# Performance work log

Hardware: AMD Instinct MI355X
Metric: run time of the kernel (lower is better)

The kernel has to match this reference:

```python
import jax, jax.numpy as jnp
import numpy as np

NUM_HEADS = 16


def spike(x):
    # forward of SpikeFunction: Heaviside step
    return (x > 0).astype(x.dtype)


def setup_inputs() -> dict:
    key = jax.random.key(0)
    ks = jax.random.split(key, 11)
    B, S, D = 2, 2048, 1024
    s = 1.0 / np.sqrt(D)
    return {
        "query": jax.random.normal(ks[0], (B, S, D), jnp.float32),
        "key": jax.random.normal(ks[1], (B, S, D), jnp.float32),
        "value": jax.random.normal(ks[2], (B, S, D), jnp.float32),
        "Wq": jax.random.normal(ks[3], (D, D), jnp.float32) * s,
        "bq": jnp.zeros((D,), jnp.float32),
        "Wk": jax.random.normal(ks[4], (D, D), jnp.float32) * s,
        "bk": jnp.zeros((D,), jnp.float32),
        "Wv": jax.random.normal(ks[5], (D, D), jnp.float32) * s,
        "bv": jnp.zeros((D,), jnp.float32),
        "Wo": jax.random.normal(ks[6], (D, D), jnp.float32) * s,
        "bo": jnp.zeros((D,), jnp.float32),
    }


def reference(query, key, value, Wq, bq, Wk, bk, Wv, bv, Wo, bo):
    B, S, D = query.shape
    H = NUM_HEADS
    hd = D // H
    # torch Linear: x @ W.T + b
    q = (query @ Wq.T + bq).reshape(B, S, H, hd).transpose(0, 2, 1, 3)
    k = (key @ Wk.T + bk).reshape(B, S, H, hd).transpose(0, 2, 1, 3)
    v = (value @ Wv.T + bv).reshape(B, S, H, hd).transpose(0, 2, 1, 3)
    scale = 1.0 / np.sqrt(hd).astype(np.float32)
    scores = jnp.einsum('bhqd,bhkd->bhqk', q, k) * scale  # [B,H,S,S]
    attn = spike(scores)  # elementwise threshold instead of softmax
    ctx = jnp.einsum('bhqk,bhkd->bhqd', attn, v)
    ctx = ctx.transpose(0, 2, 1, 3).reshape(B, S, D)
    out = ctx @ Wo.T + bo
    return out, attn
```

## Files before the change

kernel.cpp:

```cpp
#include <hip/hip_runtime.h>


#define SEQ 2048
#define DIM 1024
#define NH 16
#define HD 64
#define BATCH 2
#define MROWS (BATCH * SEQ)
#define BHT (BATCH * NH)

typedef __attribute__((ext_vector_type(8))) short short8;
typedef __attribute__((ext_vector_type(4))) float f4;
typedef unsigned short ushort;

__device__ __forceinline__ f4 mfma16(short8 a, short8 b, f4 c) {
    return __builtin_amdgcn_mfma_f32_16x16x32_bf16(a, b, c, 0, 0, 0);
}
__device__ __forceinline__ ushort rne16(float x) {
    union { float f; unsigned u; } a; a.f = x;
    return (ushort)((a.u + 0x7fffu + ((a.u >> 16) & 1u)) >> 16);
}
__device__ __forceinline__ void split2(float x, ushort& h, ushort& l) {
    union { float f; unsigned u; } a; a.f = x;
    unsigned hu = a.u & 0xffff0000u;
    h = (ushort)(hu >> 16);
    union { unsigned u; float f; } hb; hb.u = hu;
    l = rne16(x - hb.f);
}
__device__ __forceinline__ short8 ld8(const ushort* p) { return *(const short8*)p; }

__global__ __launch_bounds__(256) void wconv(const float* __restrict__ Wq,
                                             const float* __restrict__ Wk,
                                             const float* __restrict__ Wv,
                                             const float* __restrict__ Wo,
                                             ushort* __restrict__ Wqh, ushort* __restrict__ Wql,
                                             ushort* __restrict__ Wkh, ushort* __restrict__ Wkl,
                                             ushort* __restrict__ Wvb, ushort* __restrict__ Wob) {
    int i = (blockIdx.x * 256 + threadIdx.x) * 4;
    int job = blockIdx.y;
    const float* src = job == 0 ? Wq : job == 1 ? Wk : job == 2 ? Wv : Wo;
    float4 w = *(const float4*)&src[i];
    float xs[4] = {w.x, w.y, w.z, w.w};
    if (job < 2) {
        ushort h[4], l[4];
#pragma unroll
        for (int j = 0; j < 4; ++j) split2(xs[j], h[j], l[j]);
        ushort* ph = job ? Wkh : Wqh;
        ushort* pl = job ? Wkl : Wql;
        *(short4*)&ph[i] = make_short4(h[0], h[1], h[2], h[3]);
        *(short4*)&pl[i] = make_short4(l[0], l[1], l[2], l[3]);
    } else {
        ushort* po = job == 2 ? Wvb : Wob;
        *(short4*)&po[i] = make_short4(rne16(xs[0]), rne16(xs[1]), rne16(xs[2]), rne16(xs[3]));
    }
}

template <int B>
__device__ __forceinline__ void ld_qk(const float* __restrict__ X, const ushort* __restrict__ Wh,
                                      const ushort* __restrict__ Wl, int m0, int n0, int la, int qd,
                                      int k0, float4 (&xA)[2][2][2], short8 (&wH)[2][4],
                                      short8 (&wL)[2][4]) {
#pragma unroll
    for (int ms = 0; ms < 2; ++ms) {
        const float* ap = &X[(size_t)(m0 + ms * 16 + la) * DIM + k0 + qd * 8];
        xA[B][ms][0] = *(const float4*)ap;
        xA[B][ms][1] = *(const float4*)(ap + 4);
    }
#pragma unroll
    for (int ns = 0; ns < 4; ++ns) {
        size_t wi = (size_t)(n0 + ns * 16 + la) * DIM + k0 + qd * 8;
        wH[B][ns] = ld8(&Wh[wi]);
        wL[B][ns] = ld8(&Wl[wi]);
    }
}

template <int B>
__device__ __forceinline__ void fma_qk(float4 (&xA)[2][2][2], short8 (&wH)[2][4],
                                       short8 (&wL)[2][4], f4 (&acc)[2][4]) {
    short8 ahi[2], alo[2];
#pragma unroll
    for (int ms = 0; ms < 2; ++ms) {
        float xs[8] = {xA[B][ms][0].x, xA[B][ms][0].y, xA[B][ms][0].z, xA[B][ms][0].w,
                       xA[B][ms][1].x, xA[B][ms][1].y, xA[B][ms][1].z, xA[B][ms][1].w};
#pragma unroll
        for (int j = 0; j < 8; ++j) {
            ushort h, l;
            split2(xs[j], h, l);
            ahi[ms][j] = (short)h;
            alo[ms][j] = (short)l;
        }
    }
#pragma unroll
    for (int ns = 0; ns < 4; ++ns)
#pragma unroll
        for (int ms = 0; ms < 2; ++ms) {
            acc[ms][ns] = mfma16(alo[ms], wH[B][ns], acc[ms][ns]);
            acc[ms][ns] = mfma16(ahi[ms], wL[B][ns], acc[ms][ns]);
            acc[ms][ns] = mfma16(ahi[ms], wH[B][ns], acc[ms][ns]);
        }
}

template <int B>
__device__ __forceinline__ void ld_v(const float* __restrict__ X, const ushort* __restrict__ Wb,
                                     int m0, int n0, int la, int qd, int k0,
                                     float4 (&xA)[2][2][2], short8 (&wH)[2][4]) {
#pragma unroll
    for (int ms = 0; ms < 2; ++ms) {
        const float* ap = &X[(size_t)(m0 + ms * 16 + la) * DIM + k0 + qd * 8];
        xA[B][ms][0] = *(const float4*)ap;
        xA[B][ms][1] = *(const float4*)(ap + 4);
    }
#pragma unroll
    for (int ns = 0; ns < 4; ++ns)
        wH[B][ns] = ld8(&Wb[(size_t)(n0 + ns * 16 + la) * DIM + k0 + qd * 8]);
}

template <int B>
__device__ __forceinline__ void fma_v(float4 (&xA)[2][2][2], short8 (&wH)[2][4], f4 (&acc)[2][4]) {
    short8 a[2];
#pragma unroll
    for (int ms = 0; ms < 2; ++ms) {
        float xs[8] = {xA[B][ms][0].x, xA[B][ms][0].y, xA[B][ms][0].z, xA[B][ms][0].w,
                       xA[B][ms][1].x, xA[B][ms][1].y, xA[B][ms][1].z, xA[B][ms][1].w};
#pragma unroll
        for (int j = 0; j < 8; ++j) a[ms][j] = (short)rne16(xs[j]);
    }
#pragma unroll
    for (int ns = 0; ns < 4; ++ns)
#pragma unroll
        for (int ms = 0; ms < 2; ++ms) acc[ms][ns] = mfma16(a[ms], wH[B][ns], acc[ms][ns]);
}

__global__ __launch_bounds__(256, 2) void proj_qkv(
    const float* __restrict__ query, const float* __restrict__ key, const float* __restrict__ value,
    const ushort* __restrict__ Wqh, const ushort* __restrict__ Wql,
    const ushort* __restrict__ Wkh, const ushort* __restrict__ Wkl,
    const ushort* __restrict__ Wvb,
    const float* __restrict__ bq, const float* __restrict__ bk, const float* __restrict__ bv,
    ushort* __restrict__ Qhi, ushort* __restrict__ Qlo,
    ushort* __restrict__ Khi, ushort* __restrict__ Klo, ushort* __restrict__ Vt) {
    const int z = blockIdx.z;
    const int t = threadIdx.x, wave = t >> 6, lane = t & 63;
    const int la = lane & 15, qd = lane >> 4;
    const int m0 = blockIdx.x * 128 + wave * 32;
    const int n0 = blockIdx.y * 64;

    float4 xA[2][2][2];
    short8 wH[2][4], wL[2][4];
    f4 acc[2][4] = {};

    if (z < 2) {
        const float* X = z ? key : query;
        const ushort* Wh = z ? Wkh : Wqh;
        const ushort* Wl = z ? Wkl : Wql;
        ld_qk<0>(X, Wh, Wl, m0, n0, la, qd, 0, xA, wH, wL);
        for (int k0 = 0; k0 < DIM; k0 += 64) {
            ld_qk<1>(X, Wh, Wl, m0, n0, la, qd, k0 + 32, xA, wH, wL);
            fma_qk<0>(xA, wH, wL, acc);
            ld_qk<0>(X, Wh, Wl, m0, n0, la, qd, (k0 + 64) & (DIM - 1), xA, wH, wL);
            fma_qk<1>(xA, wH, wL, acc);
        }
        const float* bias = z ? bk : bq;
        ushort* Oh = z ? Khi : Qhi;
        ushort* Ol = z ? Klo : Qlo;
#pragma unroll
        for (int ns = 0; ns < 4; ++ns) {
            int n = n0 + ns * 16 + la;
            float bvv = bias[n];
            int h = n >> 6, d = n & 63;
#pragma unroll
            for (int ms = 0; ms < 2; ++ms)
#pragma unroll
                for (int r = 0; r < 4; ++r) {
                    int m = m0 + ms * 16 + qd * 4 + r;
                    int b = m >> 11, s = m & 2047;
                    ushort hh, ll;
                    split2(acc[ms][ns][r] + bvv, hh, ll);
                    size_t o = ((size_t)(b * NH + h) * SEQ + s) * HD + d;
                    Oh[o] = hh;
                    Ol[o] = ll;
                }
        }
    } else {
        __shared__ ushort Ts[4][64][40];
        ld_v<0>(value, Wvb, m0, n0, la, qd, 0, xA, wH);
        for (int k0 = 0; k0 < DIM; k0 += 64) {
            ld_v<1>(value, Wvb, m0, n0, la, qd, k0 + 32, xA, wH);
            fma_v<0>(xA, wH, acc);
            ld_v<0>(value, Wvb, m0, n0, la, qd, (k0 + 64) & (DIM - 1), xA, wH);
            fma_v<1>(xA, wH, acc);
        }
#pragma unroll
        for (int ns = 0; ns < 4; ++ns) {
            float bvv = bv[n0 + ns * 16 + la];
#pragma unroll
            for (int ms = 0; ms < 2; ++ms)
#pragma unroll
                for (int r = 0; r < 4; ++r)
                    Ts[wave][ns * 16 + la][ms * 16 + qd * 4 + r] = rne16(acc[ms][ns][r] + bvv);
        }
        int b = m0 >> 11, s0 = m0 & 2047, h = n0 >> 6;
        size_t vbase = (size_t)(b * NH + h) * HD * SEQ;
#pragma unroll
        for (int it = 0; it < 4; ++it) {
            int d = it * 16 + (lane >> 2), sc = (lane & 3) * 8;
            short8 v0 = *(const short8*)&Ts[wave][d][sc];
            *(short8*)&Vt[vbase + (size_t)d * SEQ + s0 + sc] = v0;
        }
    }
}

template <int B>
__device__ __forceinline__ void ld_at(const ushort* __restrict__ Khi, const ushort* __restrict__ Klo,
                                      const ushort* __restrict__ Vt, int bh, int c0, int la, int qd,
                                      short8 (&kH)[2][2][2], short8 (&kL)[2][2][2],
                                      short8 (&vB)[2][4]) {
#pragma unroll
    for (int n2 = 0; n2 < 2; ++n2)
#pragma unroll
        for (int ks = 0; ks < 2; ++ks) {
            size_t ki = ((size_t)bh * SEQ + c0 + n2 * 16 + la) * HD + ks * 32 + qd * 8;
            kH[B][n2][ks] = ld8(&Khi[ki]);
            kL[B][n2][ks] = ld8(&Klo[ki]);
        }
#pragma unroll
    for (int ns = 0; ns < 4; ++ns)
        vB[B][ns] = ld8(&Vt[((size_t)bh * HD + ns * 16 + la) * SEQ + c0 + qd * 8]);
}

template <int B>
__device__ __forceinline__ void half_at(ushort (*Ps)[40], float* __restrict__ attn,
                                        int bh, int q0, int c0, int wave, int lane, int la, int qd,
                                        short8 (&qhi)[2][2], short8 (&qlo)[2][2],
                                        short8 (&kH)[2][2][2], short8 (&kL)[2][2][2],
                                        short8 (&vB)[2][4], f4 (&cacc)[2][4]) {
    f4 s[2][2] = {};
#pragma unroll
    for (int n2 = 0; n2 < 2; ++n2)
#pragma unroll
        for (int ks = 0; ks < 2; ++ks)
#pragma unroll
            for (int ms = 0; ms < 2; ++ms) {
                s[ms][n2] = mfma16(qlo[ms][ks], kH[B][n2][ks], s[ms][n2]);
                s[ms][n2] = mfma16(qhi[ms][ks], kL[B][n2][ks], s[ms][n2]);
                s[ms][n2] = mfma16(qhi[ms][ks], kH[B][n2][ks], s[ms][n2]);
            }
#pragma unroll
    for (int ms = 0; ms < 2; ++ms)
#pragma unroll
        for (int n2 = 0; n2 < 2; ++n2)
#pragma unroll
            for (int r = 0; r < 4; ++r)
                Ps[wave * 32 + ms * 16 + qd * 4 + r][n2 * 16 + la] =
                    s[ms][n2][r] > 0.f ? (ushort)0x3f80 : (ushort)0;
#pragma unroll
    for (int it = 0; it < 4; ++it) {
        int row = it * 8 + (lane >> 3);
        short4 p = *(const short4*)&Ps[wave * 32 + row][(lane & 7) * 4];
        float4 o;
        o.x = __uint_as_float(((unsigned)(ushort)p.x) << 16);
        o.y = __uint_as_float(((unsigned)(ushort)p.y) << 16);
        o.z = __uint_as_float(((unsigned)(ushort)p.z) << 16);
        o.w = __uint_as_float(((unsigned)(ushort)p.w) << 16);
        *(float4*)&attn[((size_t)bh * SEQ + q0 + row) * SEQ + c0 + (lane & 7) * 4] = o;
    }
    short8 pa[2];
#pragma unroll
    for (int ms = 0; ms < 2; ++ms)
        pa[ms] = *(const short8*)&Ps[wave * 32 + ms * 16 + la][qd * 8];
#pragma unroll
    for (int ns = 0; ns < 4; ++ns)
#pragma unroll
        for (int ms = 0; ms < 2; ++ms) cacc[ms][ns] = mfma16(pa[ms], vB[B][ns], cacc[ms][ns]);
}

__global__ __launch_bounds__(256, 2) void attn_mfma(
    const ushort* __restrict__ Qhi, const ushort* __restrict__ Qlo,
    const ushort* __restrict__ Khi, const ushort* __restrict__ Klo,
    const ushort* __restrict__ Vt, float* __restrict__ attn, ushort* __restrict__ ctxb) {
    __shared__ ushort Ps[128][40];
    const int t = threadIdx.x, wave = t >> 6, lane = t & 63;
    const int la = lane & 15, qd = lane >> 4;
    const int bh = blockIdx.x;
    const int q0 = blockIdx.y * 128 + wave * 32;

    short8 qhi[2][2], qlo[2][2];
#pragma unroll
    for (int ms = 0; ms < 2; ++ms)
#pragma unroll
        for (int ks = 0; ks < 2; ++ks) {
            size_t qi = ((size_t)bh * SEQ + q0 + ms * 16 + la) * HD + ks * 32 + qd * 8;
            qhi[ms][ks] = ld8(&Qhi[qi]);
            qlo[ms][ks] = ld8(&Qlo[qi]);
        }

    short8 kH[2][2][2], kL[2][2][2], vB[2][4];
    f4 cacc[2][4] = {};
    ld_at<0>(Khi, Klo, Vt, bh, 0, la, qd, kH, kL, vB);
    for (int h = 0; h < 64; h += 2) {
        ld_at<1>(Khi, Klo, Vt, bh, (h + 1) * 32, la, qd, kH, kL, vB);
        half_at<0>(Ps, attn, bh, q0, h * 32, wave, lane, la, qd, qhi, qlo, kH, kL, vB, cacc);
        ld_at<0>(Khi, Klo, Vt, bh, ((h + 2) & 63) * 32, la, qd, kH, kL, vB);
        half_at<1>(Ps, attn, bh, q0, (h + 1) * 32, wave, lane, la, qd, qhi, qlo, kH, kL, vB, cacc);
    }
#pragma unroll
    for (int ns = 0; ns < 4; ++ns)
#pragma unroll
        for (int ms = 0; ms < 2; ++ms)
#pragma unroll
            for (int r = 0; r < 4; ++r) {
                int qrow = q0 + ms * 16 + qd * 4 + r;
                ctxb[((size_t)bh * SEQ + qrow) * HD + ns * 16 + la] = rne16(cacc[ms][ns][r]);
            }
}

template <int B>
__device__ __forceinline__ void ld_o(const ushort* __restrict__ Ctx, const ushort* __restrict__ Wb,
                                     int m0, int n0, int la, int qd, int k0,
                                     short8 (&aO)[2][2], short8 (&wO)[2][4]) {
#pragma unroll
    for (int ms = 0; ms < 2; ++ms) {
        int m = m0 + ms * 16 + la;
        int b = m >> 11, s = m & 2047;
        int k = k0 + qd * 8;
        int h = k >> 6, d = k & 63;
        aO[B][ms] = ld8(&Ctx[((size_t)(b * NH + h) * SEQ + s) * HD + d]);
    }
#pragma unroll
    for (int ns = 0; ns < 4; ++ns)
        wO[B][ns] = ld8(&Wb[(size_t)(n0 + ns * 16 + la) * DIM + k0 + qd * 8]);
}

__global__ __launch_bounds__(256, 2) void proj_out(const ushort* __restrict__ Ctx,
                                                   const ushort* __restrict__ Wb,
                                                   const float* __restrict__ bias,
                                                   float* __restrict__ out) {
    const int t = threadIdx.x, wave = t >> 6, lane = t & 63;
    const int la = lane & 15, qd = lane >> 4;
    const int m0 = blockIdx.x * 128 + wave * 32;
    const int n0 = blockIdx.y * 64;

    short8 aO[2][2], wO[2][4];
    f4 acc[2][4] = {};
    ld_o<0>(Ctx, Wb, m0, n0, la, qd, 0, aO, wO);
    for (int k0 = 0; k0 < DIM; k0 += 64) {
        ld_o<1>(Ctx, Wb, m0, n0, la, qd, k0 + 32, aO, wO);
#pragma unroll
        for (int ns = 0; ns < 4; ++ns)
#pragma unroll
            for (int ms = 0; ms < 2; ++ms) acc[ms][ns] = mfma16(aO[0][ms], wO[0][ns], acc[ms][ns]);
        ld_o<0>(Ctx, Wb, m0, n0, la, qd, (k0 + 64) & (DIM - 1), aO, wO);
#pragma unroll
        for (int ns = 0; ns < 4; ++ns)
#pragma unroll
            for (int ms = 0; ms < 2; ++ms) acc[ms][ns] = mfma16(aO[1][ms], wO[1][ns], acc[ms][ns]);
    }
#pragma unroll
    for (int ns = 0; ns < 4; ++ns) {
        int n = n0 + ns * 16 + la;
        float bvv = bias[n];
#pragma unroll
        for (int ms = 0; ms < 2; ++ms)
#pragma unroll
            for (int r = 0; r < 4; ++r) {
                int m = m0 + ms * 16 + qd * 4 + r;
                out[(size_t)m * DIM + n] = acc[ms][ns][r] + bvv;
            }
    }
}

extern "C" void kernel_launch(void* const* d_in, const int* in_sizes, int n_in,
                              void* d_out, int out_size, void* d_ws, size_t ws_size,
                              hipStream_t stream) {
    const float* query = (const float*)d_in[0];
    const float* key   = (const float*)d_in[1];
    const float* value = (const float*)d_in[2];
    const float* Wq = (const float*)d_in[3];
    const float* bq = (const float*)d_in[4];
    const float* Wk = (const float*)d_in[5];
    const float* bk = (const float*)d_in[6];
    const float* Wv = (const float*)d_in[7];
    const float* bv = (const float*)d_in[8];
    const float* Wo = (const float*)d_in[9];
    const float* bo = (const float*)d_in[10];

    float* out  = (float*)d_out;
    float* attn = out + (size_t)MROWS * DIM;

    const size_t NE = (size_t)MROWS * DIM;
    const size_t WE = (size_t)DIM * DIM;
    ushort* Qhi = (ushort*)d_ws;
    ushort* Qlo = Qhi + NE;
    ushort* Khi = Qlo + NE;
    ushort* Klo = Khi + NE;
    ushort* Vt  = Klo + NE;
    ushort* Wqh = Vt + NE;
    ushort* Wql = Wqh + WE;
    ushort* Wkh = Wql + WE;
    ushort* Wkl = Wkh + WE;
    ushort* Wvb = Wkl + WE;
    ushort* Wob = Wvb + WE;
    ushort* Ctx = Wqh;

    dim3 blk(256);
    hipLaunchKernelGGL(wconv, dim3(WE / 1024, 4), blk, 0, stream,
                       Wq, Wk, Wv, Wo, Wqh, Wql, Wkh, Wkl, Wvb, Wob);
    hipLaunchKernelGGL(proj_qkv, dim3(32, 16, 3), blk, 0, stream,
                       query, key, value, Wqh, Wql, Wkh, Wkl, Wvb, bq, bk, bv,
                       Qhi, Qlo, Khi, Klo, Vt);
    hipLaunchKernelGGL(attn_mfma, dim3(32, 16), blk, 0, stream,
                       Qhi, Qlo, Khi, Klo, Vt, attn, Ctx);
    hipLaunchKernelGGL(proj_out, dim3(32, 16), blk, 0, stream, Ctx, Wob, bo, out);
}
```

Measured before the change: 1.042 ms.

## Fuse all four stages into one persistent kernel with grid-wide barriers

Replaces the four kernels (weight conversion, QKV projection, attention, output projection) with one persistent 512-block kernel. The stages are separated by atomic-counter grid barriers that a small init kernel resets. The aim is to remove launch gaps and kernel-boundary drains. The QKV stage now runs Q, K and V sequentially in each block instead of spreading them over 1536 blocks, which lowers parallelism in that stage. The design also depends on all 512 blocks being co-resident, or the barriers deadlock.

```diff
diff --git a/kernel.cpp b/kernel.cpp
--- a/kernel.cpp
+++ b/kernel.cpp
@@ -7,7 +7,7 @@
 #define HD 64
 #define BATCH 2
 #define MROWS (BATCH * SEQ)
-#define BHT (BATCH * NH)
+#define NBLK 512
 
 typedef __attribute__((ext_vector_type(8))) short short8;
 typedef __attribute__((ext_vector_type(4))) float f4;
@@ -29,30 +29,21 @@
 }
 __device__ __forceinline__ short8 ld8(const ushort* p) { return *(const short8*)p; }
 
-__global__ __launch_bounds__(256) void wconv(const float* __restrict__ Wq,
-                                             const float* __restrict__ Wk,
-                                             const float* __restrict__ Wv,
-                                             const float* __restrict__ Wo,
-                                             ushort* __restrict__ Wqh, ushort* __restrict__ Wql,
-                                             ushort* __restrict__ Wkh, ushort* __restrict__ Wkl,
-                                             ushort* __restrict__ Wvb, ushort* __restrict__ Wob) {
-    int i = (blockIdx.x * 256 + threadIdx.x) * 4;
-    int job = blockIdx.y;
-    const float* src = job == 0 ? Wq : job == 1 ? Wk : job == 2 ? Wv : Wo;
-    float4 w = *(const float4*)&src[i];
-    float xs[4] = {w.x, w.y, w.z, w.w};
-    if (job < 2) {
-        ushort h[4], l[4];
-#pragma unroll
-        for (int j = 0; j < 4; ++j) split2(xs[j], h[j], l[j]);
-        ushort* ph = job ? Wkh : Wqh;
-        ushort* pl = job ? Wkl : Wql;
-        *(short4*)&ph[i] = make_short4(h[0], h[1], h[2], h[3]);
-        *(short4*)&pl[i] = make_short4(l[0], l[1], l[2], l[3]);
-    } else {
-        ushort* po = job == 2 ? Wvb : Wob;
-        *(short4*)&po[i] = make_short4(rne16(xs[0]), rne16(xs[1]), rne16(xs[2]), rne16(xs[3]));
-    }
+__device__ __forceinline__ void gbar(unsigned* c) {
+    __builtin_amdgcn_fence(__ATOMIC_RELEASE, "agent");
+    __syncthreads();
+    if (threadIdx.x == 0) {
+        __hip_atomic_fetch_add(c, 1u, __ATOMIC_ACQ_REL, __HIP_MEMORY_SCOPE_AGENT);
+        while (__hip_atomic_load(c, __ATOMIC_ACQUIRE, __HIP_MEMORY_SCOPE_AGENT) < NBLK) {
+            __builtin_amdgcn_s_sleep(2);
+        }
+    }
+    __syncthreads();
+    __builtin_amdgcn_fence(__ATOMIC_ACQUIRE, "agent");
+}
+
+__global__ void init_barriers(unsigned* bar) {
+    if (threadIdx.x < 8) bar[threadIdx.x] = 0;
 }
 
 template <int B>
@@ -129,85 +120,6 @@
     for (int ns = 0; ns < 4; ++ns)
 #pragma unroll
         for (int ms = 0; ms < 2; ++ms) acc[ms][ns] = mfma16(a[ms], wH[B][ns], acc[ms][ns]);
-}
-
-__global__ __launch_bounds__(256, 2) void proj_qkv(
-    const float* __restrict__ query, const float* __restrict__ key, const float* __restrict__ value,
-    const ushort* __restrict__ Wqh, const ushort* __restrict__ Wql,
-    const ushort* __restrict__ Wkh, const ushort* __restrict__ Wkl,
-    const ushort* __restrict__ Wvb,
-    const float* __restrict__ bq, const float* __restrict__ bk, const float* __restrict__ bv,
-    ushort* __restrict__ Qhi, ushort* __restrict__ Qlo,
-    ushort* __restrict__ Khi, ushort* __restrict__ Klo, ushort* __restrict__ Vt) {
-    const int z = blockIdx.z;
-    const int t = threadIdx.x, wave = t >> 6, lane = t & 63;
-    const int la = lane & 15, qd = lane >> 4;
-    const int m0 = blockIdx.x * 128 + wave * 32;
-    const int n0 = blockIdx.y * 64;
-
-    float4 xA[2][2][2];
-    short8 wH[2][4], wL[2][4];
-    f4 acc[2][4] = {};
-
-    if (z < 2) {
-        const float* X = z ? key : query;
-        const ushort* Wh = z ? Wkh : Wqh;
-        const ushort* Wl = z ? Wkl : Wql;
-        ld_qk<0>(X, Wh, Wl, m0, n0, la, qd, 0, xA, wH, wL);
-        for (int k0 = 0; k0 < DIM; k0 += 64) {
-            ld_qk<1>(X, Wh, Wl, m0, n0, la, qd, k0 + 32, xA, wH, wL);
-            fma_qk<0>(xA, wH, wL, acc);
-            ld_qk<0>(X, Wh, Wl, m0, n0, la, qd, (k0 + 64) & (DIM - 1), xA, wH, wL);
-            fma_qk<1>(xA, wH, wL, acc);
-        }
-        const float* bias = z ? bk : bq;
-        ushort* Oh = z ? Khi : Qhi;
-        ushort* Ol = z ? Klo : Qlo;
-#pragma unroll
-        for (int ns = 0; ns < 4; ++ns) {
-            int n = n0 + ns * 16 + la;
-            float bvv = bias[n];
-            int h = n >> 6, d = n & 63;
-#pragma unroll
-            for (int ms = 0; ms < 2; ++ms)
-#pragma unroll
-                for (int r = 0; r < 4; ++r) {
-                    int m = m0 + ms * 16 + qd * 4 + r;
-                    int b = m >> 11, s = m & 2047;
-                    ushort hh, ll;
-                    split2(acc[ms][ns][r] + bvv, hh, ll);
-                    size_t o = ((size_t)(b * NH + h) * SEQ + s) * HD + d;
-                    Oh[o] = hh;
-                    Ol[o] = ll;
-                }
-        }
-    } else {
-        __shared__ ushort Ts[4][64][40];
-        ld_v<0>(value, Wvb, m0, n0, la, qd, 0, xA, wH);
-        for (int k0 = 0; k0 < DIM; k0 += 64) {
-            ld_v<1>(value, Wvb, m0, n0, la, qd, k0 + 32, xA, wH);
-            fma_v<0>(xA, wH, acc);
-            ld_v<0>(value, Wvb, m0, n0, la, qd, (k0 + 64) & (DIM - 1), xA, wH);
-            fma_v<1>(xA, wH, acc);
-        }
-#pragma unroll
-        for (int ns = 0; ns < 4; ++ns) {
-            float bvv = bv[n0 + ns * 16 + la];
-#pragma unroll
-            for (int ms = 0; ms < 2; ++ms)
-#pragma unroll
-                for (int r = 0; r < 4; ++r)
-                    Ts[wave][ns * 16 + la][ms * 16 + qd * 4 + r] = rne16(acc[ms][ns][r] + bvv);
-        }
-        int b = m0 >> 11, s0 = m0 & 2047, h = n0 >> 6;
-        size_t vbase = (size_t)(b * NH + h) * HD * SEQ;
-#pragma unroll
-        for (int it = 0; it < 4; ++it) {
-            int d = it * 16 + (lane >> 2), sc = (lane & 3) * 8;
-            short8 v0 = *(const short8*)&Ts[wave][d][sc];
-            *(short8*)&Vt[vbase + (size_t)d * SEQ + s0 + sc] = v0;
-        }
-    }
 }
 
 template <int B>
@@ -274,46 +186,6 @@
         for (int ms = 0; ms < 2; ++ms) cacc[ms][ns] = mfma16(pa[ms], vB[B][ns], cacc[ms][ns]);
 }
 
-__global__ __launch_bounds__(256, 2) void attn_mfma(
-    const ushort* __restrict__ Qhi, const ushort* __restrict__ Qlo,
-    const ushort* __restrict__ Khi, const ushort* __restrict__ Klo,
-    const ushort* __restrict__ Vt, float* __restrict__ attn, ushort* __restrict__ ctxb) {
-    __shared__ ushort Ps[128][40];
-    const int t = threadIdx.x, wave = t >> 6, lane = t & 63;
-    const int la = lane & 15, qd = lane >> 4;
-    const int bh = blockIdx.x;
-    const int q0 = blockIdx.y * 128 + wave * 32;
-
-    short8 qhi[2][2], qlo[2][2];
-#pragma unroll
-    for (int ms = 0; ms < 2; ++ms)
-#pragma unroll
-        for (int ks = 0; ks < 2; ++ks) {
-            size_t qi = ((size_t)bh * SEQ + q0 + ms * 16 + la) * HD + ks * 32 + qd * 8;
-            qhi[ms][ks] = ld8(&Qhi[qi]);
-            qlo[ms][ks] = ld8(&Qlo[qi]);
-        }
-
-    short8 kH[2][2][2], kL[2][2][2], vB[2][4];
-    f4 cacc[2][4] = {};
-    ld_at<0>(Khi, Klo, Vt, bh, 0, la, qd, kH, kL, vB);
-    for (int h = 0; h < 64; h += 2) {
-        ld_at<1>(Khi, Klo, Vt, bh, (h + 1) * 32, la, qd, kH, kL, vB);
-        half_at<0>(Ps, attn, bh, q0, h * 32, wave, lane, la, qd, qhi, qlo, kH, kL, vB, cacc);
-        ld_at<0>(Khi, Klo, Vt, bh, ((h + 2) & 63) * 32, la, qd, kH, kL, vB);
-        half_at<1>(Ps, attn, bh, q0, (h + 1) * 32, wave, lane, la, qd, qhi, qlo, kH, kL, vB, cacc);
-    }
-#pragma unroll
-    for (int ns = 0; ns < 4; ++ns)
-#pragma unroll
-        for (int ms = 0; ms < 2; ++ms)
-#pragma unroll
-            for (int r = 0; r < 4; ++r) {
-                int qrow = q0 + ms * 16 + qd * 4 + r;
-                ctxb[((size_t)bh * SEQ + qrow) * HD + ns * 16 + la] = rne16(cacc[ms][ns][r]);
-            }
-}
-
 template <int B>
 __device__ __forceinline__ void ld_o(const ushort* __restrict__ Ctx, const ushort* __restrict__ Wb,
                                      int m0, int n0, int la, int qd, int k0,
@@ -331,41 +203,186 @@
         wO[B][ns] = ld8(&Wb[(size_t)(n0 + ns * 16 + la) * DIM + k0 + qd * 8]);
 }
 
-__global__ __launch_bounds__(256, 2) void proj_out(const ushort* __restrict__ Ctx,
-                                                   const ushort* __restrict__ Wb,
-                                                   const float* __restrict__ bias,
-                                                   float* __restrict__ out) {
+__global__ __launch_bounds__(256, 2) void mega(
+    const float* __restrict__ query, const float* __restrict__ key, const float* __restrict__ value,
+    const float* __restrict__ Wq, const float* __restrict__ bq,
+    const float* __restrict__ Wk, const float* __restrict__ bk,
+    const float* __restrict__ Wv, const float* __restrict__ bv,
+    const float* __restrict__ Wo, const float* __restrict__ bo,
+    float* __restrict__ out, float* __restrict__ attn,
+    ushort* __restrict__ Qhi, ushort* __restrict__ Qlo,
+    ushort* __restrict__ Khi, ushort* __restrict__ Klo,
+    ushort* __restrict__ Vt, ushort* __restrict__ Ctx,
+    ushort* __restrict__ Wqh, ushort* __restrict__ Wql,
+    ushort* __restrict__ Wkh, ushort* __restrict__ Wkl,
+    ushort* __restrict__ Wvb, ushort* __restrict__ Wob,
+    unsigned* __restrict__ bar) {
+    __shared__ ushort smem[10240];
     const int t = threadIdx.x, wave = t >> 6, lane = t & 63;
     const int la = lane & 15, qd = lane >> 4;
-    const int m0 = blockIdx.x * 128 + wave * 32;
-    const int n0 = blockIdx.y * 64;
-
-    short8 aO[2][2], wO[2][4];
-    f4 acc[2][4] = {};
-    ld_o<0>(Ctx, Wb, m0, n0, la, qd, 0, aO, wO);
-    for (int k0 = 0; k0 < DIM; k0 += 64) {
-        ld_o<1>(Ctx, Wb, m0, n0, la, qd, k0 + 32, aO, wO);
+    const int bid = blockIdx.x;
+
+    {
+#pragma unroll
+        for (int u = 0; u < 8; ++u) {
+            int unit = bid * 8 + u;
+            int mat = unit >> 10;
+            int i = (unit & 1023) * 1024 + t * 4;
+            const float* src = mat == 0 ? Wq : mat == 1 ? Wk : mat == 2 ? Wv : Wo;
+            float4 w = *(const float4*)&src[i];
+            float xs[4] = {w.x, w.y, w.z, w.w};
+            if (mat < 2) {
+                ushort h[4], l[4];
+#pragma unroll
+                for (int j = 0; j < 4; ++j) split2(xs[j], h[j], l[j]);
+                ushort* ph = mat ? Wkh : Wqh;
+                ushort* pl = mat ? Wkl : Wql;
+                *(short4*)&ph[i] = make_short4(h[0], h[1], h[2], h[3]);
+                *(short4*)&pl[i] = make_short4(l[0], l[1], l[2], l[3]);
+            } else {
+                ushort* po = mat == 2 ? Wvb : Wob;
+                *(short4*)&po[i] = make_short4(rne16(xs[0]), rne16(xs[1]), rne16(xs[2]), rne16(xs[3]));
+            }
+        }
+    }
+    gbar(bar + 0);
+
+    {
+        const int xb = bid & 31, yb = bid >> 5;
+        const int m0 = xb * 128 + wave * 32;
+        const int n0 = yb * 64;
+        float4 xA[2][2][2];
+        short8 wH[2][4], wL[2][4];
+#pragma unroll
+        for (int z = 0; z < 2; ++z) {
+            const float* X = z ? key : query;
+            const ushort* Wh = z ? Wkh : Wqh;
+            const ushort* Wl = z ? Wkl : Wql;
+            f4 acc[2][4] = {};
+            ld_qk<0>(X, Wh, Wl, m0, n0, la, qd, 0, xA, wH, wL);
+            for (int k0 = 0; k0 < DIM; k0 += 64) {
+                ld_qk<1>(X, Wh, Wl, m0, n0, la, qd, k0 + 32, xA, wH, wL);
+                fma_qk<0>(xA, wH, wL, acc);
+                ld_qk<0>(X, Wh, Wl, m0, n0, la, qd, (k0 + 64) & (DIM - 1), xA, wH, wL);
+                fma_qk<1>(xA, wH, wL, acc);
+            }
+            const float* bias = z ? bk : bq;
+            ushort* Oh = z ? Khi : Qhi;
+            ushort* Ol = z ? Klo : Qlo;
+#pragma unroll
+            for (int ns = 0; ns < 4; ++ns) {
+                int n = n0 + ns * 16 + la;
+                float bvv = bias[n];
+                int h = n >> 6, d = n & 63;
+#pragma unroll
+                for (int ms = 0; ms < 2; ++ms)
+#pragma unroll
+                    for (int r = 0; r < 4; ++r) {
+                        int m = m0 + ms * 16 + qd * 4 + r;
+                        int b = m >> 11, s = m & 2047;
+                        ushort hh, ll;
+                        split2(acc[ms][ns][r] + bvv, hh, ll);
+                        size_t o = ((size_t)(b * NH + h) * SEQ + s) * HD + d;
+                        Oh[o] = hh;
+                        Ol[o] = ll;
+                    }
+            }
+        }
+        {
+            ushort(*Ts)[64][40] = (ushort(*)[64][40])smem;
+            f4 acc[2][4] = {};
+            ld_v<0>(value, Wvb, m0, n0, la, qd, 0, xA, wH);
+            for (int k0 = 0; k0 < DIM; k0 += 64) {
+                ld_v<1>(value, Wvb, m0, n0, la, qd, k0 + 32, xA, wH);
+                fma_v<0>(xA, wH, acc);
+                ld_v<0>(value, Wvb, m0, n0, la, qd, (k0 + 64) & (DIM - 1), xA, wH);
+                fma_v<1>(xA, wH, acc);
+            }
+#pragma unroll
+            for (int ns = 0; ns < 4; ++ns) {
+                float bvv = bv[n0 + ns * 16 + la];
+#pragma unroll
+                for (int ms = 0; ms < 2; ++ms)
+#pragma unroll
+                    for (int r = 0; r < 4; ++r)
+                        Ts[wave][ns * 16 + la][ms * 16 + qd * 4 + r] = rne16(acc[ms][ns][r] + bvv);
+            }
+            int b = m0 >> 11, s0 = m0 & 2047, h = n0 >> 6;
+            size_t vbase = (size_t)(b * NH + h) * HD * SEQ;
+#pragma unroll
+            for (int it = 0; it < 4; ++it) {
+                int d = it * 16 + (lane >> 2), sc = (lane & 3) * 8;
+                short8 v0 = *(const short8*)&Ts[wave][d][sc];
+                *(short8*)&Vt[vbase + (size_t)d * SEQ + s0 + sc] = v0;
+            }
+        }
+    }
+    gbar(bar + 1);
+
+    {
+        ushort(*Ps)[40] = (ushort(*)[40])smem;
+        const int bh = bid & 31;
+        const int q0 = (bid >> 5) * 128 + wave * 32;
+        short8 qhi[2][2], qlo[2][2];
+#pragma unroll
+        for (int ms = 0; ms < 2; ++ms)
+#pragma unroll
+            for (int ks = 0; ks < 2; ++ks) {
+                size_t qi = ((size_t)bh * SEQ + q0 + ms * 16 + la) * HD + ks * 32 + qd * 8;
+                qhi[ms][ks] = ld8(&Qhi[qi]);
+                qlo[ms][ks] = ld8(&Qlo[qi]);
+            }
+        short8 kH[2][2][2], kL[2][2][2], vB[2][4];
+        f4 cacc[2][4] = {};
+        ld_at<0>(Khi, Klo, Vt, bh, 0, la, qd, kH, kL, vB);
+        for (int h = 0; h < 64; h += 2) {
+            ld_at<1>(Khi, Klo, Vt, bh, (h + 1) * 32, la, qd, kH, kL, vB);
+            half_at<0>(Ps, attn, bh, q0, h * 32, wave, lane, la, qd, qhi, qlo, kH, kL, vB, cacc);
+            ld_at<0>(Khi, Klo, Vt, bh, ((h + 2) & 63) * 32, la, qd, kH, kL, vB);
+            half_at<1>(Ps, attn, bh, q0, (h + 1) * 32, wave, lane, la, qd, qhi, qlo, kH, kL, vB, cacc);
+        }
 #pragma unroll
         for (int ns = 0; ns < 4; ++ns)
 #pragma unroll
-            for (int ms = 0; ms < 2; ++ms) acc[ms][ns] = mfma16(aO[0][ms], wO[0][ns], acc[ms][ns]);
-        ld_o<0>(Ctx, Wb, m0, n0, la, qd, (k0 + 64) & (DIM - 1), aO, wO);
-#pragma unroll
-        for (int ns = 0; ns < 4; ++ns)
-#pragma unroll
-            for (int ms = 0; ms < 2; ++ms) acc[ms][ns] = mfma16(aO[1][ms], wO[1][ns], acc[ms][ns]);
-    }
-#pragma unroll
-    for (int ns = 0; ns < 4; ++ns) {
-        int n = n0 + ns * 16 + la;
-        float bvv = bias[n];
-#pragma unroll
-        for (int ms = 0; ms < 2; ++ms)
-#pragma unroll
-            for (int r = 0; r < 4; ++r) {
-                int m = m0 + ms * 16 + qd * 4 + r;
-                out[(size_t)m * DIM + n] = acc[ms][ns][r] + bvv;
-            }
+            for (int ms = 0; ms < 2; ++ms)
+#pragma unroll
+                for (int r = 0; r < 4; ++r) {
+                    int qrow = q0 + ms * 16 + qd * 4 + r;
+                    Ctx[((size_t)bh * SEQ + qrow) * HD + ns * 16 + la] = rne16(cacc[ms][ns][r]);
+                }
+    }
+    gbar(bar + 2);
+
+    {
+        const int m0 = (bid & 31) * 128 + wave * 32;
+        const int n0 = (bid >> 5) * 64;
+        short8 aO[2][2], wO[2][4];
+        f4 acc[2][4] = {};
+        ld_o<0>(Ctx, Wob, m0, n0, la, qd, 0, aO, wO);
+        for (int k0 = 0; k0 < DIM; k0 += 64) {
+            ld_o<1>(Ctx, Wob, m0, n0, la, qd, k0 + 32, aO, wO);
+#pragma unroll
+            for (int ns = 0; ns < 4; ++ns)
+#pragma unroll
+                for (int ms = 0; ms < 2; ++ms) acc[ms][ns] = mfma16(aO[0][ms], wO[0][ns], acc[ms][ns]);
+            ld_o<0>(Ctx, Wob, m0, n0, la, qd, (k0 + 64) & (DIM - 1), aO, wO);
+#pragma unroll
+            for (int ns = 0; ns < 4; ++ns)
+#pragma unroll
+                for (int ms = 0; ms < 2; ++ms) acc[ms][ns] = mfma16(aO[1][ms], wO[1][ns], acc[ms][ns]);
+        }
+#pragma unroll
+        for (int ns = 0; ns < 4; ++ns) {
+            int n = n0 + ns * 16 + la;
+            float bvv = bo[n];
+#pragma unroll
+            for (int ms = 0; ms < 2; ++ms)
+#pragma unroll
+                for (int r = 0; r < 4; ++r) {
+                    int m = m0 + ms * 16 + qd * 4 + r;
+                    out[(size_t)m * DIM + n] = acc[ms][ns][r] + bvv;
+                }
+        }
     }
 }
 
@@ -401,14 +418,11 @@
     ushort* Wvb = Wkl + WE;
     ushort* Wob = Wvb + WE;
     ushort* Ctx = Wqh;
-
-    dim3 blk(256);
-    hipLaunchKernelGGL(wconv, dim3(WE / 1024, 4), blk, 0, stream,
-                       Wq, Wk, Wv, Wo, Wqh, Wql, Wkh, Wkl, Wvb, Wob);
-    hipLaunchKernelGGL(proj_qkv, dim3(32, 16, 3), blk, 0, stream,
-                       query, key, value, Wqh, Wql, Wkh, Wkl, Wvb, bq, bk, bv,
-                       Qhi, Qlo, Khi, Klo, Vt);
-    hipLaunchKernelGGL(attn_mfma, dim3(32, 16), blk, 0, stream,
-                       Qhi, Qlo, Khi, Klo, Vt, attn, Ctx);
-    hipLaunchKernelGGL(proj_out, dim3(32, 16), blk, 0, stream, Ctx, Wob, bo, out);
-}
+    unsigned* bar = (unsigned*)(Wob + WE);
+
+    hipLaunchKernelGGL(init_barriers, dim3(1), dim3(64), 0, stream, bar);
+    hipLaunchKernelGGL(mega, dim3(NBLK), dim3(256), 0, stream,
+                       query, key, value, Wq, bq, Wk, bk, Wv, bv, Wo, bo,
+                       out, attn, Qhi, Qlo, Khi, Klo, Vt, Ctx,
+                       Wqh, Wql, Wkh, Wkl, Wvb, Wob, bar);
+}
```

Result: slower. 1.712 ms (+64.3%).
